# Performance work log

Measured on AMD Instinct MI355X. Metric: run time of the kernel, lower is better.

The kernel has to match this reference:

```python
import jax, jax.numpy as jnp
import numpy as np

B, DIN, N = 4096, 1024, 1024

def _hard_sigmoid(z):
    # Keras hard_sigmoid: clip(0.2*x + 0.5, 0, 1)
    return jnp.clip(0.2 * z + 0.5, 0.0, 1.0)

def setup_inputs() -> dict:
    key = jax.random.key(0)
    ks = jax.random.split(key, 12)
    s_in = 1.0 / np.sqrt(DIN)
    s_h = 1.0 / np.sqrt(N)
    d = {
        'x': jax.random.normal(ks[0], (B, DIN), jnp.float32),
        'c0': jax.random.normal(ks[1], (B, N), jnp.float32),
        'h0': jax.random.normal(ks[2], (B, N), jnp.float32),
        'Wf': jax.random.normal(ks[3], (DIN, N), jnp.float32) * s_in,
        'Wi': jax.random.normal(ks[4], (DIN, N), jnp.float32) * s_in,
        'Wo': jax.random.normal(ks[5], (DIN, N), jnp.float32) * s_in,
        'Wc': jax.random.normal(ks[6], (DIN, N), jnp.float32) * s_in,
        'Uf': jax.random.normal(ks[7], (N, N), jnp.float32) * s_h,
        'Ui': jax.random.normal(ks[8], (N, N), jnp.float32) * s_h,
        'Uo': jax.random.normal(ks[9], (N, N), jnp.float32) * s_h,
        'Uc': jax.random.normal(ks[10], (N, N), jnp.float32) * s_h,
        'bf': jnp.zeros((N,), jnp.float32),
        'bi': jnp.zeros((N,), jnp.float32),
        'bo': jnp.zeros((N,), jnp.float32),
        'bc': jnp.zeros((N,), jnp.float32),
    }
    return d

def reference(x, c0, h0, Wf, Wi, Wo, Wc, Uf, Ui, Uo, Uc, bf, bi, bo, bc):
    # Fuse the 8 small Dense ops into two GEMMs on concatenated weights
    W = jnp.concatenate([Wf, Wi, Wo, Wc], axis=1)            # [DIN, 4N]
    U = jnp.concatenate([Uf, Ui, Uo, Uc], axis=1)            # [N, 4N]
    b = jnp.concatenate([bf, bi, bo, bc], axis=0)            # [4N]
    z = x @ W + h0 @ U + b                                   # [B, 4N]
    zf, zi, zo, zc = jnp.split(z, 4, axis=1)
    f = _hard_sigmoid(zf)
    i = _hard_sigmoid(zi)
    o = _hard_sigmoid(zo)
    c_tilde = jnp.tanh(zc)
    c = f * c0 + i * c_tilde
    h = o * jnp.tanh(c)
    return (h, c, h)  # (output, new_c, new_h)
```

## Files before the change

### kernel.cpp

```cpp
#include <hip/hip_runtime.h>
#include <hip/hip_bf16.h>
#include <stdint.h>

typedef unsigned short u16;
typedef __attribute__((ext_vector_type(8))) short short8;
typedef __attribute__((ext_vector_type(4))) float f32x4;

#define BATCH 4096
#define DIN   1024
#define NH    1024
#define KTOT  2048
#define BM    128
#define BN    32
#define BK    64

__device__ __forceinline__ void gload_lds16(const void* gp, void* lp) {
    __builtin_amdgcn_global_load_lds(
        (const __attribute__((address_space(1))) uint32_t*)gp,
        (__attribute__((address_space(3))) uint32_t*)lp, 16, 0, 0);
}

__device__ __forceinline__ u16 f2bf(float f) {
    uint32_t t; __builtin_memcpy(&t, &f, 4);
    uint32_t r = (t + 0x7FFFu + ((t >> 16) & 1u)) >> 16;
    return (u16)r;
}
__device__ __forceinline__ float hsig(float z) {
    return fminf(fmaxf(fmaf(z, 0.2f, 0.5f), 0.0f), 1.0f);
}
__device__ __forceinline__ float fast_tanh(float x) {
    x = fminf(fmaxf(x, -12.0f), 12.0f);
    float e = __expf(2.0f * x);
    return (e - 1.0f) / (e + 1.0f);
}

__global__ __launch_bounds__(256) void acast_kernel(
    const float* __restrict__ x, const float* __restrict__ h0,
    u16* __restrict__ Abuf)
{
    const int c  = blockIdx.x * 256 + threadIdx.x;
    const int m  = c >> 8;
    const int kc = (c & 255) * 8;
    const float* src = (kc < DIN) ? (x + (size_t)m * DIN + kc)
                                  : (h0 + (size_t)m * DIN + (kc - DIN));
    float4 v0 = *(const float4*)(src);
    float4 v1 = *(const float4*)(src + 4);
    union { u16 v[8]; uint4 q; } pk;
    pk.v[0] = f2bf(v0.x); pk.v[1] = f2bf(v0.y);
    pk.v[2] = f2bf(v0.z); pk.v[3] = f2bf(v0.w);
    pk.v[4] = f2bf(v1.x); pk.v[5] = f2bf(v1.y);
    pk.v[6] = f2bf(v1.z); pk.v[7] = f2bf(v1.w);
    *(uint4*)(Abuf + (size_t)m * KTOT + kc) = pk.q;
}

__global__ __launch_bounds__(256) void wtrans_kernel(
    const float* __restrict__ Wf, const float* __restrict__ Wi,
    const float* __restrict__ Wo, const float* __restrict__ Wc,
    const float* __restrict__ Uf, const float* __restrict__ Ui,
    const float* __restrict__ Uo, const float* __restrict__ Uc,
    u16* __restrict__ Bt)
{
    __shared__ u16 tile[64][65];
    const int mz = blockIdx.z;
    const float* srcs[8] = {Wf, Wi, Wo, Wc, Uf, Ui, Uo, Uc};
    const float* src = srcs[mz];
    const int g    = mz & 3;
    const int koff = (mz >> 2) << 10;
    const int k0 = blockIdx.x * 64;
    const int n0 = blockIdx.y * 64;
    const int tid = threadIdx.x;

#pragma unroll
    for (int i = 0; i < 4; i++) {
        int idx = i * 256 + tid;
        int kk = idx >> 4, c = idx & 15;
        float4 v = *(const float4*)(src + (size_t)(k0 + kk) * NH + n0 + c * 4);
        u16* dst = &tile[kk][c * 4];
        dst[0] = f2bf(v.x); dst[1] = f2bf(v.y);
        dst[2] = f2bf(v.z); dst[3] = f2bf(v.w);
    }
    __syncthreads();
#pragma unroll
    for (int i = 0; i < 2; i++) {
        int idx = i * 256 + tid;
        int nn = idx >> 3, c = idx & 7;
        union { u16 v[8]; uint4 q; } pk;
#pragma unroll
        for (int j = 0; j < 8; j++) pk.v[j] = tile[c * 8 + j][nn];
        *(uint4*)(Bt + ((size_t)(g * NH + n0 + nn)) * KTOT + koff + k0 + c * 8) = pk.q;
    }
}

__global__ __launch_bounds__(256, 2) void lstm_gemm_kernel(
    const u16* __restrict__ Abuf, const float* __restrict__ c0,
    const u16* __restrict__ Bt,
    const float* __restrict__ bfv, const float* __restrict__ biv,
    const float* __restrict__ bov, const float* __restrict__ bcv,
    float* __restrict__ out)
{
    __shared__ u16 As[BM * BK];
    __shared__ u16 Bs[4 * BN * BK];

    const int tid  = threadIdx.x;
    const int wv   = tid >> 6;
    const int lane = tid & 63;
    const int m0 = blockIdx.x * BM;
    const int n0 = blockIdx.y * BN;

    const int lr  = lane >> 3;
    const int lcs = ((lane & 7) ^ lr) * 8;

    f32x4 acc[2][4][2];
#pragma unroll
    for (int mt = 0; mt < 2; mt++)
#pragma unroll
        for (int g = 0; g < 4; g++)
#pragma unroll
            for (int nt = 0; nt < 2; nt++)
                acc[mt][g][nt] = (f32x4){0.f, 0.f, 0.f, 0.f};

    const int am   = lane & 15;
    const int am7  = am & 7;
    const int quad = lane >> 4;

    for (int k0 = 0; k0 < KTOT; k0 += BK) {
#pragma unroll
        for (int j = 0; j < 4; j++) {
            int r = (wv * 4 + j) * 8 + lr;
            gload_lds16(Abuf + (size_t)(m0 + r) * KTOT + k0 + lcs,
                        (void*)(As + (wv * 4 + j) * 512));
        }
#pragma unroll
        for (int j = 0; j < 4; j++) {
            int rowIdx = (wv * 4 + j) * 8 + lr;
            int grow = (rowIdx >> 5) * NH + n0 + (rowIdx & 31);
            gload_lds16(Bt + (size_t)grow * KTOT + k0 + lcs,
                        (void*)(Bs + (wv * 4 + j) * 512));
        }
        __syncthreads();
#pragma unroll
        for (int ks = 0; ks < 2; ks++) {
            const int sw = (((ks * 4 + quad) ^ am7) << 3);
            short8 a0 = *(const short8*)(As + (wv * 32 +      am) * BK + sw);
            short8 a1 = *(const short8*)(As + (wv * 32 + 16 + am) * BK + sw);
#pragma unroll
            for (int g = 0; g < 4; g++) {
#pragma unroll
                for (int nt = 0; nt < 2; nt++) {
                    short8 b = *(const short8*)(Bs + (g * 32 + nt * 16 + am) * BK + sw);
                    acc[0][g][nt] = __builtin_amdgcn_mfma_f32_16x16x32_bf16(a0, b, acc[0][g][nt], 0, 0, 0);
                    acc[1][g][nt] = __builtin_amdgcn_mfma_f32_16x16x32_bf16(a1, b, acc[1][g][nt], 0, 0, 0);
                }
            }
        }
        __syncthreads();
    }

    float bias[4][2];
    const float* bptr[4] = {bfv, biv, bov, bcv};
#pragma unroll
    for (int g = 0; g < 4; g++)
#pragma unroll
        for (int nt = 0; nt < 2; nt++)
            bias[g][nt] = bptr[g][n0 + nt * 16 + am];

    const size_t HN = (size_t)BATCH * NH;
#pragma unroll
    for (int mt = 0; mt < 2; mt++) {
#pragma unroll
        for (int r = 0; r < 4; r++) {
            const int row = m0 + wv * 32 + mt * 16 + quad * 4 + r;
#pragma unroll
            for (int nt = 0; nt < 2; nt++) {
                const int col = n0 + nt * 16 + am;
                const size_t off = (size_t)row * NH + col;
                float zf = acc[mt][0][nt][r] + bias[0][nt];
                float zi = acc[mt][1][nt][r] + bias[1][nt];
                float zo = acc[mt][2][nt][r] + bias[2][nt];
                float zc = acc[mt][3][nt][r] + bias[3][nt];
                float fg = hsig(zf), ig = hsig(zi), og = hsig(zo);
                float ct = fast_tanh(zc);
                float cn = fg * c0[off] + ig * ct;
                float hn = og * fast_tanh(cn);
                out[off]            = hn;
                out[HN + off]       = cn;
                out[2 * HN + off]   = hn;
            }
        }
    }
}

extern "C" void kernel_launch(void* const* d_in, const int* in_sizes, int n_in,
                              void* d_out, int out_size, void* d_ws, size_t ws_size,
                              hipStream_t stream) {
    const float* x  = (const float*)d_in[0];
    const float* c0 = (const float*)d_in[1];
    const float* h0 = (const float*)d_in[2];
    const float* Wf = (const float*)d_in[3];
    const float* Wi = (const float*)d_in[4];
    const float* Wo = (const float*)d_in[5];
    const float* Wc = (const float*)d_in[6];
    const float* Uf = (const float*)d_in[7];
    const float* Ui = (const float*)d_in[8];
    const float* Uo = (const float*)d_in[9];
    const float* Uc = (const float*)d_in[10];
    const float* bf = (const float*)d_in[11];
    const float* bi = (const float*)d_in[12];
    const float* bo = (const float*)d_in[13];
    const float* bc = (const float*)d_in[14];

    u16* Bt   = (u16*)d_ws;
    u16* Abuf = (u16*)d_ws + (size_t)4 * NH * KTOT;

    acast_kernel<<<(BATCH * KTOT / 8) / 256, 256, 0, stream>>>(x, h0, Abuf);

    dim3 tg(1024 / 64, 1024 / 64, 8);
    wtrans_kernel<<<tg, 256, 0, stream>>>(Wf, Wi, Wo, Wc, Uf, Ui, Uo, Uc, Bt);

    dim3 gg(BATCH / BM, NH / BN);
    lstm_gemm_kernel<<<gg, 256, 0, stream>>>(Abuf, c0, Bt, bf, bi, bo, bc,
                                             (float*)d_out);
}
```

Before: 216.3 us.

## Switch GEMM to 32x32x16 MFMA with two waves per block

Replaces the 16x16x32 bf16 MFMA tiling with 32x32x16 MFMA, so each wave now covers 64 rows × 32 cols × 4 gates. The block shrinks to 128 threads (2 waves), and each thread issues twice as many LDS loads. The larger MFMA cuts LDS fragment reads per FLOP and the instruction count. In exchange, per-wave accumulator registers grow, latency hiding with fewer waves per block may suffer, and the epilogue row mapping changes to the 32x32 output layout.

```diff
diff --git a/kernel.cpp b/kernel.cpp
--- a/kernel.cpp
+++ b/kernel.cpp
@@ -4,7 +4,7 @@
 
 typedef unsigned short u16;
 typedef __attribute__((ext_vector_type(8))) short short8;
-typedef __attribute__((ext_vector_type(4))) float f32x4;
+typedef __attribute__((ext_vector_type(16))) float f32x16;
 
 #define BATCH 4096
 #define DIN   1024
@@ -91,7 +91,7 @@
     }
 }
 
-__global__ __launch_bounds__(256, 2) void lstm_gemm_kernel(
+__global__ __launch_bounds__(128, 2) void lstm_gemm_kernel(
     const u16* __restrict__ Abuf, const float* __restrict__ c0,
     const u16* __restrict__ Bt,
     const float* __restrict__ bfv, const float* __restrict__ biv,
@@ -110,82 +110,71 @@
     const int lr  = lane >> 3;
     const int lcs = ((lane & 7) ^ lr) * 8;
 
-    f32x4 acc[2][4][2];
+    f32x16 acc[2][4];
 #pragma unroll
     for (int mt = 0; mt < 2; mt++)
 #pragma unroll
         for (int g = 0; g < 4; g++)
 #pragma unroll
-            for (int nt = 0; nt < 2; nt++)
-                acc[mt][g][nt] = (f32x4){0.f, 0.f, 0.f, 0.f};
-
-    const int am   = lane & 15;
-    const int am7  = am & 7;
-    const int quad = lane >> 4;
+            for (int e = 0; e < 16; e++)
+                acc[mt][g][e] = 0.f;
+
+    const int an   = lane & 31;
+    const int an7  = lane & 7;
+    const int half = lane >> 5;
 
     for (int k0 = 0; k0 < KTOT; k0 += BK) {
 #pragma unroll
-        for (int j = 0; j < 4; j++) {
-            int r = (wv * 4 + j) * 8 + lr;
+        for (int j = 0; j < 8; j++) {
+            int r = (wv * 8 + j) * 8 + lr;
             gload_lds16(Abuf + (size_t)(m0 + r) * KTOT + k0 + lcs,
-                        (void*)(As + (wv * 4 + j) * 512));
-        }
-#pragma unroll
-        for (int j = 0; j < 4; j++) {
-            int rowIdx = (wv * 4 + j) * 8 + lr;
+                        (void*)(As + (wv * 8 + j) * 512));
+        }
+#pragma unroll
+        for (int j = 0; j < 8; j++) {
+            int rowIdx = (wv * 8 + j) * 8 + lr;
             int grow = (rowIdx >> 5) * NH + n0 + (rowIdx & 31);
             gload_lds16(Bt + (size_t)grow * KTOT + k0 + lcs,
-                        (void*)(Bs + (wv * 4 + j) * 512));
+                        (void*)(Bs + (wv * 8 + j) * 512));
         }
         __syncthreads();
 #pragma unroll
-        for (int ks = 0; ks < 2; ks++) {
-            const int sw = (((ks * 4 + quad) ^ am7) << 3);
-            short8 a0 = *(const short8*)(As + (wv * 32 +      am) * BK + sw);
-            short8 a1 = *(const short8*)(As + (wv * 32 + 16 + am) * BK + sw);
+        for (int ks = 0; ks < 4; ks++) {
+            const int sw = (((ks * 2 + half) ^ an7) << 3);
+            short8 a0 = *(const short8*)(As + (wv * 64 +      an) * BK + sw);
+            short8 a1 = *(const short8*)(As + (wv * 64 + 32 + an) * BK + sw);
 #pragma unroll
             for (int g = 0; g < 4; g++) {
-#pragma unroll
-                for (int nt = 0; nt < 2; nt++) {
-                    short8 b = *(const short8*)(Bs + (g * 32 + nt * 16 + am) * BK + sw);
-                    acc[0][g][nt] = __builtin_amdgcn_mfma_f32_16x16x32_bf16(a0, b, acc[0][g][nt], 0, 0, 0);
-                    acc[1][g][nt] = __builtin_amdgcn_mfma_f32_16x16x32_bf16(a1, b, acc[1][g][nt], 0, 0, 0);
-                }
+                short8 b = *(const short8*)(Bs + (g * 32 + an) * BK + sw);
+                acc[0][g] = __builtin_amdgcn_mfma_f32_32x32x16_bf16(a0, b, acc[0][g], 0, 0, 0);
+                acc[1][g] = __builtin_amdgcn_mfma_f32_32x32x16_bf16(a1, b, acc[1][g], 0, 0, 0);
             }
         }
         __syncthreads();
     }
 
-    float bias[4][2];
-    const float* bptr[4] = {bfv, biv, bov, bcv};
-#pragma unroll
-    for (int g = 0; g < 4; g++)
-#pragma unroll
-        for (int nt = 0; nt < 2; nt++)
-            bias[g][nt] = bptr[g][n0 + nt * 16 + am];
+    const int col = n0 + an;
+    float bias0 = bfv[col], bias1 = biv[col], bias2 = bov[col], bias3 = bcv[col];
 
     const size_t HN = (size_t)BATCH * NH;
 #pragma unroll
     for (int mt = 0; mt < 2; mt++) {
 #pragma unroll
-        for (int r = 0; r < 4; r++) {
-            const int row = m0 + wv * 32 + mt * 16 + quad * 4 + r;
-#pragma unroll
-            for (int nt = 0; nt < 2; nt++) {
-                const int col = n0 + nt * 16 + am;
-                const size_t off = (size_t)row * NH + col;
-                float zf = acc[mt][0][nt][r] + bias[0][nt];
-                float zi = acc[mt][1][nt][r] + bias[1][nt];
-                float zo = acc[mt][2][nt][r] + bias[2][nt];
-                float zc = acc[mt][3][nt][r] + bias[3][nt];
-                float fg = hsig(zf), ig = hsig(zi), og = hsig(zo);
-                float ct = fast_tanh(zc);
-                float cn = fg * c0[off] + ig * ct;
-                float hn = og * fast_tanh(cn);
-                out[off]            = hn;
-                out[HN + off]       = cn;
-                out[2 * HN + off]   = hn;
-            }
+        for (int reg = 0; reg < 16; reg++) {
+            const int row = m0 + wv * 64 + mt * 32 +
+                            (reg & 3) + 8 * (reg >> 2) + 4 * half;
+            const size_t off = (size_t)row * NH + col;
+            float zf = acc[mt][0][reg] + bias0;
+            float zi = acc[mt][1][reg] + bias1;
+            float zo = acc[mt][2][reg] + bias2;
+            float zc = acc[mt][3][reg] + bias3;
+            float fg = hsig(zf), ig = hsig(zi), og = hsig(zo);
+            float ct = fast_tanh(zc);
+            float cn = fg * c0[off] + ig * ct;
+            float hn = og * fast_tanh(cn);
+            out[off]            = hn;
+            out[HN + off]       = cn;
+            out[2 * HN + off]   = hn;
         }
     }
 }
@@ -218,6 +207,6 @@
     wtrans_kernel<<<tg, 256, 0, stream>>>(Wf, Wi, Wo, Wc, Uf, Ui, Uo, Uc, Bt);
 
     dim3 gg(BATCH / BM, NH / BN);
-    lstm_gemm_kernel<<<gg, 256, 0, stream>>>(Abuf, c0, Bt, bf, bi, bo, bc,
+    lstm_gemm_kernel<<<gg, 128, 0, stream>>>(Abuf, c0, Bt, bf, bi, bo, bc,
                                              (float*)d_out);
 }
```

After: 227.8 us. 1.05x slower.
